# Performance work log

Hardware: AMD Instinct MI355X
Metric: run time of the kernel (lower is better)

The kernel has to match this reference:

```python
import jax, jax.numpy as jnp
import numpy as np

N_ENTRIES = 4_194_304   # total CSR entries (gene observations)
H, W = 256, 256
N_PIXELS = H * W
N_GENES = 30000
FEATURE_DIM = 64


def setup_inputs() -> dict:
    key = jax.random.key(0)
    k1, k2, k3, k4 = jax.random.split(key, 4)
    # gene id per CSR entry
    indices = jax.random.randint(k1, (N_ENTRIES,), 0, N_GENES, dtype=jnp.int64)
    # counts per entry (positive floats)
    cnts = jax.random.uniform(k2, (N_ENTRIES,), dtype=jnp.float32) * 10.0
    # CSR row pointers over pixels: sorted, starting at 0, ending at N_ENTRIES
    indptr = jnp.sort(jax.random.randint(k3, (N_PIXELS + 1,), 0, N_ENTRIES + 1, dtype=jnp.int64))
    indptr = indptr.at[0].set(0).at[-1].set(N_ENTRIES)
    # params: gamma init zeros, tokens variance_scaling(1.0,'fan_in','normal',out_axis=0)
    gamma = jnp.zeros((N_GENES,), jnp.float32)
    tokens = jax.random.normal(k4, (N_GENES, FEATURE_DIM), dtype=jnp.float32) * (1.0 / np.sqrt(FEATURE_DIM))
    return {"indices": indices, "cnts": cnts, "indptr": indptr, "gamma": gamma, "tokens": tokens}


def reference(indices, cnts, indptr, gamma, tokens):
    # SGStem with rescale=True, normalize=False (module defaults)
    n_entries = indices.shape[0]
    n_pixels = indptr.shape[0] - 1  # == H*W
    # mask padding entries beyond indptr[-1]
    valid = jnp.arange(n_entries) < indptr[-1]
    c = jnp.where(valid, cnts, 0.0)
    # rescale counts by per-gene exp(gamma)
    c = c * jnp.exp(gamma[indices])
    # CSR -> segment ids per entry
    rpt = jnp.diff(indptr)
    segms = jnp.repeat(jnp.arange(n_pixels), rpt, total_repeat_length=n_entries)
    # gather token embeddings, scale, scatter-add into pixel bins
    embeddings = tokens[indices] * c[:, None]  # (n_entries, feature_dim)
    embedding_sum = jax.ops.segment_sum(embeddings, segms, num_segments=n_pixels)
    return embedding_sum.reshape(H, W, tokens.shape[-1])
```

## Files before the change

### kernel.cpp

```cpp
#include <hip/hip_runtime.h>
#include <hip/hip_bf16.h>

#define FDIM 64
#define N_PIXELS 65536
#define N_ENTRIES 4194304
#define WAVES_PER_BLOCK 2
#define EPW 256
#define N_WAVES (N_ENTRIES / EPW)
#define PAD 64

typedef unsigned int u32;
typedef u32 u32x4 __attribute__((ext_vector_type(4)));

__device__ __forceinline__ unsigned short f32_to_bf16_rne(float f) {
    unsigned int u = __float_as_uint(f);
    u = (u + 0x7FFFu + ((u >> 16) & 1u)) >> 16;
    return (unsigned short)u;
}

__global__ __launch_bounds__(256) void convert_tokens(
    const float4* __restrict__ tokens4,
    const float* __restrict__ gamma,
    ushort4* __restrict__ tok_bf)
{
    const int i = blockIdx.x * blockDim.x + threadIdx.x;
    const int g = i >> 4;
    const float eg = __expf(gamma[g]);
    const float4 t = tokens4[i];
    ushort4 o;
    o.x = f32_to_bf16_rne(t.x * eg);
    o.y = f32_to_bf16_rne(t.y * eg);
    o.z = f32_to_bf16_rne(t.z * eg);
    o.w = f32_to_bf16_rne(t.w * eg);
    tok_bf[i] = o;
}

__global__ __launch_bounds__(WAVES_PER_BLOCK * 64, 4) void sgstem_main(
    const int* __restrict__ indices,
    const float* __restrict__ cnts,
    const int* __restrict__ indptr,
    const char* __restrict__ tokp,
    float* __restrict__ out)
{
    __shared__ int2 meta[WAVES_PER_BLOCK][EPW + PAD];

    const int lane = threadIdx.x & 63;
    const int wave = threadIdx.x >> 6;
    const int g    = lane >> 3;
    const int fl   = lane & 7;
    const int flb  = fl * 16;

    const int wid = __builtin_amdgcn_readfirstlane(
        blockIdx.x * WAVES_PER_BLOCK + wave);
    const int e0 = wid * EPW;
    const int e1 = e0 + EPW;

    #pragma unroll
    for (int c = 0; c < EPW / 64; ++c) {
        const int e = e0 + c * 64 + lane;
        const int   idx = indices[e];
        const float cnt = cnts[e];
        meta[wave][c * 64 + lane] = make_int2(idx * 128, __float_as_int(cnt));
    }
    meta[wave][EPW + lane] = make_int2(0, 0);

    int lo = 0, hi = N_PIXELS;
    while (lo < hi) {
        const int mid = (lo + hi + 1) >> 1;
        if (indptr[mid] <= e0) lo = mid; else hi = mid - 1;
    }
    int p = lo;

    #define GLOAD(dst, off) \
        asm volatile("global_load_dwordx4 %0, %1, %2" \
                     : "=v"(dst) : "v"(off), "s"(tokp) : "memory")
    #define CONSUME(tk, sc) \
        a0 = fmaf(__uint_as_float(tk.x << 16),         sc, a0); \
        a1 = fmaf(__uint_as_float(tk.x & 0xFFFF0000u), sc, a1); \
        a2 = fmaf(__uint_as_float(tk.y << 16),         sc, a2); \
        a3 = fmaf(__uint_as_float(tk.y & 0xFFFF0000u), sc, a3); \
        a4 = fmaf(__uint_as_float(tk.z << 16),         sc, a4); \
        a5 = fmaf(__uint_as_float(tk.z & 0xFFFF0000u), sc, a5); \
        a6 = fmaf(__uint_as_float(tk.w << 16),         sc, a6); \
        a7 = fmaf(__uint_as_float(tk.w & 0xFFFF0000u), sc, a7)

    while (p < N_PIXELS) {
        const int ps = indptr[p];
        if (ps >= e1) break;
        const int pe = indptr[p + 1];
        const int s = max(ps, e0);
        const int t = min(pe, e1);

        if (t > s) {
            const int r0 = s - e0;
            const int r1 = t - e0;

            float a0 = 0.f, a1 = 0.f, a2 = 0.f, a3 = 0.f;
            float a4 = 0.f, a5 = 0.f, a6 = 0.f, a7 = 0.f;

            int rb = r0;
            for (; rb + 64 <= r1; rb += 64) {
                const int q = rb + g;
                const int2 m0 = meta[wave][q];
                const int2 m1 = meta[wave][q + 8];
                const int2 m2 = meta[wave][q + 16];
                const int2 m3 = meta[wave][q + 24];
                const int2 m4 = meta[wave][q + 32];
                const int2 m5 = meta[wave][q + 40];
                const int2 m6 = meta[wave][q + 48];
                const int2 m7 = meta[wave][q + 56];

                u32x4 t0, t1, t2, t3, t4, t5, t6, t7;
                GLOAD(t0, m0.x + flb); GLOAD(t1, m1.x + flb);
                GLOAD(t2, m2.x + flb); GLOAD(t3, m3.x + flb);
                GLOAD(t4, m4.x + flb); GLOAD(t5, m5.x + flb);
                GLOAD(t6, m6.x + flb); GLOAD(t7, m7.x + flb);

                const float s0 = __int_as_float(m0.y);
                const float s1 = __int_as_float(m1.y);
                const float s2 = __int_as_float(m2.y);
                const float s3 = __int_as_float(m3.y);
                const float s4 = __int_as_float(m4.y);
                const float s5 = __int_as_float(m5.y);
                const float s6 = __int_as_float(m6.y);
                const float s7 = __int_as_float(m7.y);

                asm volatile("s_waitcnt vmcnt(4)" ::: "memory");
                __builtin_amdgcn_sched_barrier(0);
                CONSUME(t0, s0); CONSUME(t1, s1); CONSUME(t2, s2); CONSUME(t3, s3);
                asm volatile("s_waitcnt vmcnt(0)" ::: "memory");
                __builtin_amdgcn_sched_barrier(0);
                CONSUME(t4, s4); CONSUME(t5, s5); CONSUME(t6, s6); CONSUME(t7, s7);
            }

            if (rb < r1) {
                const int q = rb + g;
                const int2 m0 = meta[wave][q];
                const int2 m1 = meta[wave][q + 8];
                const int2 m2 = meta[wave][q + 16];
                const int2 m3 = meta[wave][q + 24];
                const int2 m4 = meta[wave][q + 32];
                const int2 m5 = meta[wave][q + 40];
                const int2 m6 = meta[wave][q + 48];
                const int2 m7 = meta[wave][q + 56];

                const int o0 = ((q      < r1) ? m0.x : 0) + flb;
                const int o1 = ((q +  8 < r1) ? m1.x : 0) + flb;
                const int o2 = ((q + 16 < r1) ? m2.x : 0) + flb;
                const int o3 = ((q + 24 < r1) ? m3.x : 0) + flb;
                const int o4 = ((q + 32 < r1) ? m4.x : 0) + flb;
                const int o5 = ((q + 40 < r1) ? m5.x : 0) + flb;
                const int o6 = ((q + 48 < r1) ? m6.x : 0) + flb;
                const int o7 = ((q + 56 < r1) ? m7.x : 0) + flb;

                u32x4 t0, t1, t2, t3, t4, t5, t6, t7;
                GLOAD(t0, o0); GLOAD(t1, o1); GLOAD(t2, o2); GLOAD(t3, o3);
                GLOAD(t4, o4); GLOAD(t5, o5); GLOAD(t6, o6); GLOAD(t7, o7);

                const float s0 = (q      < r1) ? __int_as_float(m0.y) : 0.f;
                const float s1 = (q +  8 < r1) ? __int_as_float(m1.y) : 0.f;
                const float s2 = (q + 16 < r1) ? __int_as_float(m2.y) : 0.f;
                const float s3 = (q + 24 < r1) ? __int_as_float(m3.y) : 0.f;
                const float s4 = (q + 32 < r1) ? __int_as_float(m4.y) : 0.f;
                const float s5 = (q + 40 < r1) ? __int_as_float(m5.y) : 0.f;
                const float s6 = (q + 48 < r1) ? __int_as_float(m6.y) : 0.f;
                const float s7 = (q + 56 < r1) ? __int_as_float(m7.y) : 0.f;

                asm volatile("s_waitcnt vmcnt(4)" ::: "memory");
                __builtin_amdgcn_sched_barrier(0);
                CONSUME(t0, s0); CONSUME(t1, s1); CONSUME(t2, s2); CONSUME(t3, s3);
                asm volatile("s_waitcnt vmcnt(0)" ::: "memory");
                __builtin_amdgcn_sched_barrier(0);
                CONSUME(t4, s4); CONSUME(t5, s5); CONSUME(t6, s6); CONSUME(t7, s7);
            }

            #pragma unroll
            for (int mask = 8; mask <= 32; mask <<= 1) {
                a0 += __shfl_xor(a0, mask);
                a1 += __shfl_xor(a1, mask);
                a2 += __shfl_xor(a2, mask);
                a3 += __shfl_xor(a3, mask);
                a4 += __shfl_xor(a4, mask);
                a5 += __shfl_xor(a5, mask);
                a6 += __shfl_xor(a6, mask);
                a7 += __shfl_xor(a7, mask);
            }

            if (g == 0) {
                const bool interior = (ps >= e0) && (pe <= e1);
                if (interior) {
                    float4* o4 = (float4*)(out + p * FDIM);
                    o4[fl * 2]     = make_float4(a0, a1, a2, a3);
                    o4[fl * 2 + 1] = make_float4(a4, a5, a6, a7);
                } else {
                    float* o = out + p * FDIM + fl * 8;
                    atomicAdd(o + 0, a0);
                    atomicAdd(o + 1, a1);
                    atomicAdd(o + 2, a2);
                    atomicAdd(o + 3, a3);
                    atomicAdd(o + 4, a4);
                    atomicAdd(o + 5, a5);
                    atomicAdd(o + 6, a6);
                    atomicAdd(o + 7, a7);
                }
            }
        }
        ++p;
    }
    #undef GLOAD
    #undef CONSUME
}

extern "C" void kernel_launch(void* const* d_in, const int* in_sizes, int n_in,
                              void* d_out, int out_size, void* d_ws, size_t ws_size,
                              hipStream_t stream) {
    const int*    indices = (const int*)d_in[0];
    const float*  cnts    = (const float*)d_in[1];
    const int*    indptr  = (const int*)d_in[2];
    const float*  gamma   = (const float*)d_in[3];
    const float4* tokens4 = (const float4*)d_in[4];
    float*        out     = (float*)d_out;

    ushort4* tok_bf = (ushort4*)d_ws;

    hipMemsetAsync(d_out, 0, (size_t)N_PIXELS * FDIM * sizeof(float), stream);

    convert_tokens<<<1875, 256, 0, stream>>>(tokens4, gamma, tok_bf);

    sgstem_main<<<N_WAVES / WAVES_PER_BLOCK, WAVES_PER_BLOCK * 64, 0, stream>>>(
        indices, cnts, indptr, (const char*)tok_bf, out);
}
```

Baseline: 169.7 us.

## Precompute per-wave start pixels in a separate kernel and use one-wave blocks with larger chunks

```diff
diff --git a/kernel.cpp b/kernel.cpp
--- a/kernel.cpp
+++ b/kernel.cpp
@@ -4,8 +4,7 @@
 #define FDIM 64
 #define N_PIXELS 65536
 #define N_ENTRIES 4194304
-#define WAVES_PER_BLOCK 2
-#define EPW 256
+#define EPW 512
 #define N_WAVES (N_ENTRIES / EPW)
 #define PAD 64
 
@@ -35,23 +34,36 @@
     tok_bf[i] = o;
 }
 
-__global__ __launch_bounds__(WAVES_PER_BLOCK * 64, 4) void sgstem_main(
+__global__ __launch_bounds__(64) void search_starts(
+    const int* __restrict__ indptr,
+    int* __restrict__ p0arr)
+{
+    const int w = blockIdx.x * 64 + threadIdx.x;
+    const int e0 = w * EPW;
+    int lo = 0, hi = N_PIXELS;
+    while (lo < hi) {
+        const int mid = (lo + hi + 1) >> 1;
+        if (indptr[mid] <= e0) lo = mid; else hi = mid - 1;
+    }
+    p0arr[w] = lo;
+}
+
+__global__ __launch_bounds__(64, 4) void sgstem_main(
     const int* __restrict__ indices,
     const float* __restrict__ cnts,
     const int* __restrict__ indptr,
     const char* __restrict__ tokp,
+    const int* __restrict__ p0arr,
     float* __restrict__ out)
 {
-    __shared__ int2 meta[WAVES_PER_BLOCK][EPW + PAD];
-
-    const int lane = threadIdx.x & 63;
-    const int wave = threadIdx.x >> 6;
+    __shared__ int2 meta[EPW + PAD];
+
+    const int lane = threadIdx.x;
     const int g    = lane >> 3;
     const int fl   = lane & 7;
     const int flb  = fl * 16;
 
-    const int wid = __builtin_amdgcn_readfirstlane(
-        blockIdx.x * WAVES_PER_BLOCK + wave);
+    const int wid = __builtin_amdgcn_readfirstlane(blockIdx.x);
     const int e0 = wid * EPW;
     const int e1 = e0 + EPW;
 
@@ -60,16 +72,11 @@
         const int e = e0 + c * 64 + lane;
         const int   idx = indices[e];
         const float cnt = cnts[e];
-        meta[wave][c * 64 + lane] = make_int2(idx * 128, __float_as_int(cnt));
+        meta[c * 64 + lane] = make_int2(idx * 128, __float_as_int(cnt));
     }
-    meta[wave][EPW + lane] = make_int2(0, 0);
-
-    int lo = 0, hi = N_PIXELS;
-    while (lo < hi) {
-        const int mid = (lo + hi + 1) >> 1;
-        if (indptr[mid] <= e0) lo = mid; else hi = mid - 1;
-    }
-    int p = lo;
+    meta[EPW + lane] = make_int2(0, 0);
+
+    int p = p0arr[wid];
 
     #define GLOAD(dst, off) \
         asm volatile("global_load_dwordx4 %0, %1, %2" \
@@ -101,14 +108,14 @@
             int rb = r0;
             for (; rb + 64 <= r1; rb += 64) {
                 const int q = rb + g;
-                const int2 m0 = meta[wave][q];
-                const int2 m1 = meta[wave][q + 8];
-                const int2 m2 = meta[wave][q + 16];
-                const int2 m3 = meta[wave][q + 24];
-                const int2 m4 = meta[wave][q + 32];
-                const int2 m5 = meta[wave][q + 40];
-                const int2 m6 = meta[wave][q + 48];
-                const int2 m7 = meta[wave][q + 56];
+                const int2 m0 = meta[q];
+                const int2 m1 = meta[q + 8];
+                const int2 m2 = meta[q + 16];
+                const int2 m3 = meta[q + 24];
+                const int2 m4 = meta[q + 32];
+                const int2 m5 = meta[q + 40];
+                const int2 m6 = meta[q + 48];
+                const int2 m7 = meta[q + 56];
 
                 u32x4 t0, t1, t2, t3, t4, t5, t6, t7;
                 GLOAD(t0, m0.x + flb); GLOAD(t1, m1.x + flb);
@@ -135,14 +142,14 @@
 
             if (rb < r1) {
                 const int q = rb + g;
-                const int2 m0 = meta[wave][q];
-                const int2 m1 = meta[wave][q + 8];
-                const int2 m2 = meta[wave][q + 16];
-                const int2 m3 = meta[wave][q + 24];
-                const int2 m4 = meta[wave][q + 32];
-                const int2 m5 = meta[wave][q + 40];
-                const int2 m6 = meta[wave][q + 48];
-                const int2 m7 = meta[wave][q + 56];
+                const int2 m0 = meta[q];
+                const int2 m1 = meta[q + 8];
+                const int2 m2 = meta[q + 16];
+                const int2 m3 = meta[q + 24];
+                const int2 m4 = meta[q + 32];
+                const int2 m5 = meta[q + 40];
+                const int2 m6 = meta[q + 48];
+                const int2 m7 = meta[q + 56];
 
                 const int o0 = ((q      < r1) ? m0.x : 0) + flb;
                 const int o1 = ((q +  8 < r1) ? m1.x : 0) + flb;
@@ -221,12 +228,14 @@
     const float4* tokens4 = (const float4*)d_in[4];
     float*        out     = (float*)d_out;
 
-    ushort4* tok_bf = (ushort4*)d_ws;
+    int*     p0arr  = (int*)d_ws;
+    ushort4* tok_bf = (ushort4*)((char*)d_ws + 32768);
 
     hipMemsetAsync(d_out, 0, (size_t)N_PIXELS * FDIM * sizeof(float), stream);
 
     convert_tokens<<<1875, 256, 0, stream>>>(tokens4, gamma, tok_bf);
-
-    sgstem_main<<<N_WAVES / WAVES_PER_BLOCK, WAVES_PER_BLOCK * 64, 0, stream>>>(
-        indices, cnts, indptr, (const char*)tok_bf, out);
-}
+    search_starts<<<N_WAVES / 64, 64, 0, stream>>>(indptr, p0arr);
+
+    sgstem_main<<<N_WAVES, 64, 0, stream>>>(
+        indices, cnts, indptr, (const char*)tok_bf, p0arr, out);
+}
```

Result: faster. 153.1 us (-9.8%).
